# Optimization experiments

Measured on AMD Instinct MI355X. Metric: run time of the kernel, lower is better.

The kernel has to match this reference:

```python
import jax, jax.numpy as jnp
import numpy as np

N_CHUNKS = 4 * 28  # hardcoded 112 chunks in the original; chunk sizes are equal when N % 112 == 0


def setup_inputs() -> dict:
    key = jax.random.key(0)
    k1, k2, k3 = jax.random.split(key, 3)
    b, d, h, w = 8, 512, 28, 28  # N = b*h*w = 6272, divisible by 112
    x = jax.random.normal(k1, (b, d, h, w), dtype=jnp.float32)
    p_mu = jax.random.normal(k2, (b * h * w, d), dtype=jnp.float32)
    p_logvar = jax.random.normal(k3, (b * h * w, d), dtype=jnp.float32)
    return {"x": x, "p_mu": p_mu, "p_logvar": p_logvar}


def _club_loss(x, p_mu, p_logvar):
    # (b, d, h, w) -> (N, d) with N = b*h*w
    b, d, h, w = x.shape
    flat_x = jnp.transpose(x, (0, 2, 3, 1)).reshape(-1, d)  # (N, d)

    inv_ev = jnp.exp(-p_logvar)  # (N, d)

    # positive[i] = -0.5 * sum_d (x_i - mu_i)^2 / exp(logvar_i)
    positive = -0.5 * jnp.sum(jnp.square(flat_x - p_mu) * inv_ev, axis=-1)  # (N,)

    # negative[i] = -0.5 * mean_j sum_d (x_j - mu_i)^2 / exp(logvar_i)
    # Expand the square so the j-contraction becomes GEMMs (no (N,N,d) intermediate):
    #   D[i,j] = <x_j^2, inv_ev_i> - 2 <x_j, mu_i * inv_ev_i> + <mu_i^2, inv_ev_i>
    x2 = jnp.square(flat_x)                                   # (N, d)
    term_x2 = jnp.einsum('id,jd->ij', inv_ev, x2)             # (N_i, N_j)
    term_cross = jnp.einsum('id,jd->ij', p_mu * inv_ev, flat_x)
    term_mu2 = jnp.sum(jnp.square(p_mu) * inv_ev, axis=-1, keepdims=True)  # (N_i, 1)
    D = term_x2 - 2.0 * term_cross + term_mu2                 # (N_i, N_j)
    negative = -0.5 * jnp.mean(D, axis=1)                     # (N,)

    # Original averages each of the 112 equal-size chunks then averages the
    # chunk means, which equals the global mean for equal chunk sizes.
    return jnp.mean(positive - negative)


def reference(x, p_mu, p_logvar):
    return _club_loss(x, p_mu, p_logvar)
```

## Files before the change

### kernel.cpp

```cpp
#include <hip/hip_runtime.h>


#define Dd   512
#define HWs  784
#define Nn   6272
#define LSx  260


__global__ __launch_bounds__(256) void club_main(
    const float* __restrict__ x, const float* __restrict__ p_mu,
    const float* __restrict__ p_lv, float* __restrict__ ws)
{
    __shared__ __align__(16) float smem[16 * LSx + 16];

    const int t   = threadIdx.x;
    const int bid = blockIdx.x;
    const int ct  = bid & 1;
    const int ht  = (bid >> 1) % 49;
    const int b   = bid / 98;
    const int c0  = ct * 256;
    const int hw0 = ht * 16;
    const int rep = (bid >> 1) & 7;

    const int dx = t >> 2;
    const int g  = t & 3;
    const float* xb = x + ((size_t)(b * Dd + c0 + dx) * HWs + hw0 + 4 * g);
    const float4 x0 = *(const float4*)(xb);
    const float4 x1 = *(const float4*)(xb +  64 * HWs);
    const float4 x2 = *(const float4*)(xb + 128 * HWs);
    const float4 x3 = *(const float4*)(xb + 192 * HWs);

    const int r0 = b * HWs + hw0;
    const size_t mbase = (size_t)(r0 + (t >> 6)) * Dd + c0 + 4 * (t & 63);
    const float* mp = p_mu + mbase;
    const float* lp = p_lv + mbase;
    const float4 m0 = *(const float4*)(mp);
    const float4 m1 = *(const float4*)(mp + 2048);
    const float4 m2 = *(const float4*)(mp + 4096);
    const float4 m3 = *(const float4*)(mp + 6144);
    const float4 l0 = *(const float4*)(lp);
    const float4 l1 = *(const float4*)(lp + 2048);
    const float4 l2 = *(const float4*)(lp + 4096);
    const float4 l3 = *(const float4*)(lp + 6144);

    {
        const int rr = 4 * g;
#define XST(V, K) do {                                                \
        const int c = dx + 64 * (K);                                  \
        smem[(rr + 0) * LSx + c] = (V).x;                             \
        smem[(rr + 1) * LSx + c] = (V).y;                             \
        smem[(rr + 2) * LSx + c] = (V).z;                             \
        smem[(rr + 3) * LSx + c] = (V).w;                             \
    } while (0)
        XST(x0, 0); XST(x1, 1); XST(x2, 2); XST(x3, 3);
#undef XST
    }
    __syncthreads();

    float4 aI = {0,0,0,0}, aM = {0,0,0,0}, sX = {0,0,0,0}, sX2 = {0,0,0,0};
    float aP = 0.f, aM2 = 0.f;
    const int cc = 4 * (t & 63);
    const int rb = t >> 6;

#define ACC1(XV, MU, LV, F) do {                                      \
        const float iev = __expf(-(LV).F);                            \
        const float dd  = (XV).F - (MU).F;                            \
        aP += dd * dd * iev;                                          \
        aI.F += iev;                                                  \
        const float mi = (MU).F * iev;                                \
        aM.F += mi; aM2 += (MU).F * mi;                               \
        sX.F += (XV).F; sX2.F += (XV).F * (XV).F;                     \
    } while (0)
#define ACCROW(K, MU, LV) do {                                        \
        const float4 xv = *(const float4*)&smem[(rb + 4 * (K)) * LSx + cc]; \
        ACC1(xv, MU, LV, x); ACC1(xv, MU, LV, y);                     \
        ACC1(xv, MU, LV, z); ACC1(xv, MU, LV, w);                     \
    } while (0)
    ACCROW(0, m0, l0); ACCROW(1, m1, l1); ACCROW(2, m2, l2); ACCROW(3, m3, l3);
#undef ACCROW
#undef ACC1

    float4* red4 = (float4*)smem;
    float4 rI, rM, rX, rX2;
#define COLRED(SRC, DST) do {                                         \
        __syncthreads();                                              \
        red4[t] = (SRC);                                              \
        __syncthreads();                                              \
        if (t < 128) { float4 o = red4[t + 128];                      \
            red4[t].x += o.x; red4[t].y += o.y;                       \
            red4[t].z += o.z; red4[t].w += o.w; }                     \
        __syncthreads();                                              \
        if (t < 64) { float4 a = red4[t], o = red4[t + 64];           \
            (DST).x = a.x + o.x; (DST).y = a.y + o.y;                 \
            (DST).z = a.z + o.z; (DST).w = a.w + o.w; }               \
    } while (0)
    COLRED(aI, rI); COLRED(aM, rM); COLRED(sX, rX); COLRED(sX2, rX2);
#undef COLRED

#pragma unroll
    for (int off = 32; off > 0; off >>= 1) {
        aP  += __shfl_down(aP,  off);
        aM2 += __shfl_down(aM2, off);
    }
    __syncthreads();
    if ((t & 63) == 0) {
        smem[16 * LSx + (t >> 6)]     = aP;
        smem[16 * LSx + 8 + (t >> 6)] = aM2;
    }
    __syncthreads();

    if (t < 64) {
        const int c = c0 + 4 * t;
        float* wi = ws +         rep * Dd + c;
        float* wm = ws +  4096 + rep * Dd + c;
        float* wx = ws +  8192 + rep * Dd + c;
        float* w2 = ws + 12288 + rep * Dd + c;
        atomicAdd(wi + 0, rI.x); atomicAdd(wi + 1, rI.y);
        atomicAdd(wi + 2, rI.z); atomicAdd(wi + 3, rI.w);
        atomicAdd(wm + 0, rM.x); atomicAdd(wm + 1, rM.y);
        atomicAdd(wm + 2, rM.z); atomicAdd(wm + 3, rM.w);
        atomicAdd(wx + 0, rX.x); atomicAdd(wx + 1, rX.y);
        atomicAdd(wx + 2, rX.z); atomicAdd(wx + 3, rX.w);
        atomicAdd(w2 + 0, rX2.x); atomicAdd(w2 + 1, rX2.y);
        atomicAdd(w2 + 2, rX2.z); atomicAdd(w2 + 3, rX2.w);
    }
    if (t == 0) {
        double* wd = (double*)((char*)ws + 65536);
        atomicAdd(wd + rep, (double)(smem[16*LSx+0] + smem[16*LSx+1]
                                   + smem[16*LSx+2] + smem[16*LSx+3]));
        atomicAdd(wd + 8 + rep, (double)(smem[16*LSx+8] + smem[16*LSx+9]
                                       + smem[16*LSx+10] + smem[16*LSx+11]));
    }
}

__global__ __launch_bounds__(256) void club_fin(
    const float* __restrict__ ws, float* __restrict__ out)
{
    __shared__ double red[256];
    const int t = threadIdx.x;
    double acc = 0.0;
    for (int c = t; c < Dd; c += 256) {
        float inv = 0.f, muv = 0.f, sx = 0.f, sx2 = 0.f;
#pragma unroll
        for (int r = 0; r < 8; ++r) {
            inv += ws[r * Dd + c];
            muv += ws[4096 + r * Dd + c];
            sx  += ws[8192 + r * Dd + c];
            sx2 += ws[12288 + r * Dd + c];
        }
        acc += (double)sx2 * (double)inv - 2.0 * (double)sx * (double)muv;
    }
    red[t] = acc; __syncthreads();
    for (int s = 128; s > 0; s >>= 1) {
        if (t < s) red[t] += red[t + s];
        __syncthreads();
    }
    if (t == 0) {
        const double* wd = (const double*)((const char*)ws + 65536);
        double P = 0.0, M2 = 0.0;
#pragma unroll
        for (int r = 0; r < 8; ++r) { P += wd[r]; M2 += wd[8 + r]; }
        const double sumD = red[0] + (double)Nn * M2;
        out[0] = (float)((-0.5 / (double)Nn) * P
                       + (0.5 / ((double)Nn * (double)Nn)) * sumD);
    }
}

extern "C" void kernel_launch(void* const* d_in, const int* in_sizes, int n_in,
                              void* d_out, int out_size, void* d_ws, size_t ws_size,
                              hipStream_t stream) {
    const float* x    = (const float*)d_in[0];
    const float* p_mu = (const float*)d_in[1];
    const float* p_lv = (const float*)d_in[2];
    float* ws = (float*)d_ws;

    hipMemsetAsync(d_ws, 0, 65536 + 128, stream);

    club_main<<<784, 256, 0, stream>>>(x, p_mu, p_lv, ws);
    club_fin<<<1, 256, 0, stream>>>(ws, (float*)d_out);
}
```

Measured before the change: 102.3 us.

## Fuse finalize into main kernel via last-block counter and halve block count

Merges the separate finalize kernel into the main kernel: each block bumps an atomic counter after its partial sums, and the last block to finish runs the final reduction and writes the output. Each block now covers both channel halves for a 16-pixel tile, giving 392 blocks instead of 784 with double the loads in flight per thread. This removes one kernel launch and its dependency gap, at the cost of more registers and LDS per block and a serialized tail in the last block.

```diff
diff --git a/kernel.cpp b/kernel.cpp
--- a/kernel.cpp
+++ b/kernel.cpp
@@ -5,96 +5,119 @@
 #define HWs  784
 #define Nn   6272
 #define LSx  260
-
-
-__global__ __launch_bounds__(256) void club_main(
+#define NBLK 392
+
+
+__global__ __launch_bounds__(256) void club_all(
     const float* __restrict__ x, const float* __restrict__ p_mu,
-    const float* __restrict__ p_lv, float* __restrict__ ws)
+    const float* __restrict__ p_lv, float* __restrict__ ws,
+    float* __restrict__ out)
 {
-    __shared__ __align__(16) float smem[16 * LSx + 16];
+    __shared__ __align__(16) float smem[2 * 16 * LSx];
+    __shared__ float sbuf[16];
+    __shared__ int lastFlag;
 
     const int t   = threadIdx.x;
-    const int bid = blockIdx.x;
-    const int ct  = bid & 1;
-    const int ht  = (bid >> 1) % 49;
-    const int b   = bid / 98;
-    const int c0  = ct * 256;
+    const int j   = blockIdx.x;
+    const int b   = j / 49;
+    const int ht  = j % 49;
     const int hw0 = ht * 16;
-    const int rep = (bid >> 1) & 7;
-
-    const int dx = t >> 2;
-    const int g  = t & 3;
-    const float* xb = x + ((size_t)(b * Dd + c0 + dx) * HWs + hw0 + 4 * g);
-    const float4 x0 = *(const float4*)(xb);
-    const float4 x1 = *(const float4*)(xb +  64 * HWs);
-    const float4 x2 = *(const float4*)(xb + 128 * HWs);
-    const float4 x3 = *(const float4*)(xb + 192 * HWs);
-
-    const int r0 = b * HWs + hw0;
-    const size_t mbase = (size_t)(r0 + (t >> 6)) * Dd + c0 + 4 * (t & 63);
-    const float* mp = p_mu + mbase;
-    const float* lp = p_lv + mbase;
-    const float4 m0 = *(const float4*)(mp);
-    const float4 m1 = *(const float4*)(mp + 2048);
-    const float4 m2 = *(const float4*)(mp + 4096);
-    const float4 m3 = *(const float4*)(mp + 6144);
-    const float4 l0 = *(const float4*)(lp);
-    const float4 l1 = *(const float4*)(lp + 2048);
-    const float4 l2 = *(const float4*)(lp + 4096);
-    const float4 l3 = *(const float4*)(lp + 6144);
-
-    {
-        const int rr = 4 * g;
-#define XST(V, K) do {                                                \
-        const int c = dx + 64 * (K);                                  \
-        smem[(rr + 0) * LSx + c] = (V).x;                             \
-        smem[(rr + 1) * LSx + c] = (V).y;                             \
-        smem[(rr + 2) * LSx + c] = (V).z;                             \
-        smem[(rr + 3) * LSx + c] = (V).w;                             \
-    } while (0)
-        XST(x0, 0); XST(x1, 1); XST(x2, 2); XST(x3, 3);
+    const int r0  = b * HWs + hw0;
+    const int rep = j & 7;
+
+    const int dx = t >> 2, g = t & 3;
+    const float* xb0 = x + ((size_t)(b * Dd + dx) * HWs + hw0 + 4 * g);
+    const float4 A0 = *(const float4*)(xb0);
+    const float4 A1 = *(const float4*)(xb0 +  64 * HWs);
+    const float4 A2 = *(const float4*)(xb0 + 128 * HWs);
+    const float4 A3 = *(const float4*)(xb0 + 192 * HWs);
+    const float* xb1 = xb0 + 256 * HWs;
+    const float4 B0 = *(const float4*)(xb1);
+    const float4 B1 = *(const float4*)(xb1 +  64 * HWs);
+    const float4 B2 = *(const float4*)(xb1 + 128 * HWs);
+    const float4 B3 = *(const float4*)(xb1 + 192 * HWs);
+
+    const size_t mb0 = (size_t)(r0 + (t >> 6)) * Dd + 4 * (t & 63);
+    const float4 M00 = *(const float4*)(p_mu + mb0);
+    const float4 M01 = *(const float4*)(p_mu + mb0 + 2048);
+    const float4 M02 = *(const float4*)(p_mu + mb0 + 4096);
+    const float4 M03 = *(const float4*)(p_mu + mb0 + 6144);
+    const float4 L00 = *(const float4*)(p_lv + mb0);
+    const float4 L01 = *(const float4*)(p_lv + mb0 + 2048);
+    const float4 L02 = *(const float4*)(p_lv + mb0 + 4096);
+    const float4 L03 = *(const float4*)(p_lv + mb0 + 6144);
+
+#define XST(V, HALF, K) do {                                           \
+        const int c_ = dx + 64 * (K);                                  \
+        float* s_ = smem + (HALF) * 16 * LSx + (4 * g) * LSx + c_;     \
+        s_[0 * LSx] = (V).x; s_[1 * LSx] = (V).y;                      \
+        s_[2 * LSx] = (V).z; s_[3 * LSx] = (V).w;                      \
+    } while (0)
+    XST(A0, 0, 0); XST(A1, 0, 1); XST(A2, 0, 2); XST(A3, 0, 3);
+    XST(B0, 1, 0); XST(B1, 1, 1); XST(B2, 1, 2); XST(B3, 1, 3);
 #undef XST
-    }
-    __syncthreads();
-
-    float4 aI = {0,0,0,0}, aM = {0,0,0,0}, sX = {0,0,0,0}, sX2 = {0,0,0,0};
-    float aP = 0.f, aM2 = 0.f;
+
+    const size_t mb1 = mb0 + 256;
+    const float4 M10 = *(const float4*)(p_mu + mb1);
+    const float4 M11 = *(const float4*)(p_mu + mb1 + 2048);
+    const float4 M12 = *(const float4*)(p_mu + mb1 + 4096);
+    const float4 M13 = *(const float4*)(p_mu + mb1 + 6144);
+    const float4 L10 = *(const float4*)(p_lv + mb1);
+    const float4 L11 = *(const float4*)(p_lv + mb1 + 2048);
+    const float4 L12 = *(const float4*)(p_lv + mb1 + 4096);
+    const float4 L13 = *(const float4*)(p_lv + mb1 + 6144);
+
+    __syncthreads();
+
     const int cc = 4 * (t & 63);
     const int rb = t >> 6;
-
-#define ACC1(XV, MU, LV, F) do {                                      \
-        const float iev = __expf(-(LV).F);                            \
-        const float dd  = (XV).F - (MU).F;                            \
-        aP += dd * dd * iev;                                          \
-        aI.F += iev;                                                  \
-        const float mi = (MU).F * iev;                                \
-        aM.F += mi; aM2 += (MU).F * mi;                               \
-        sX.F += (XV).F; sX2.F += (XV).F * (XV).F;                     \
-    } while (0)
-#define ACCROW(K, MU, LV) do {                                        \
-        const float4 xv = *(const float4*)&smem[(rb + 4 * (K)) * LSx + cc]; \
-        ACC1(xv, MU, LV, x); ACC1(xv, MU, LV, y);                     \
-        ACC1(xv, MU, LV, z); ACC1(xv, MU, LV, w);                     \
-    } while (0)
-    ACCROW(0, m0, l0); ACCROW(1, m1, l1); ACCROW(2, m2, l2); ACCROW(3, m3, l3);
+    float4 aI0 = {0,0,0,0}, aM0 = {0,0,0,0}, sX0 = {0,0,0,0}, s20 = {0,0,0,0};
+    float4 aI1 = {0,0,0,0}, aM1 = {0,0,0,0}, sX1 = {0,0,0,0}, s21 = {0,0,0,0};
+    float aP = 0.f, aM2 = 0.f;
+
+#define ACC1(XV, MU, LV, F, AI, AM, SX, S2) do {                       \
+        const float iev = __expf(-(LV).F);                             \
+        const float dd  = (XV).F - (MU).F;                             \
+        aP += dd * dd * iev;                                           \
+        (AI).F += iev;                                                 \
+        const float mi = (MU).F * iev;                                 \
+        (AM).F += mi; aM2 += (MU).F * mi;                              \
+        (SX).F += (XV).F; (S2).F += (XV).F * (XV).F;                   \
+    } while (0)
+#define ACCROW(HALF, K, MU, LV, AI, AM, SX, S2) do {                   \
+        const float4 xv = *(const float4*)&smem[(HALF)*16*LSx + (rb + 4*(K))*LSx + cc]; \
+        ACC1(xv, MU, LV, x, AI, AM, SX, S2);                           \
+        ACC1(xv, MU, LV, y, AI, AM, SX, S2);                           \
+        ACC1(xv, MU, LV, z, AI, AM, SX, S2);                           \
+        ACC1(xv, MU, LV, w, AI, AM, SX, S2);                           \
+    } while (0)
+    ACCROW(0, 0, M00, L00, aI0, aM0, sX0, s20);
+    ACCROW(0, 1, M01, L01, aI0, aM0, sX0, s20);
+    ACCROW(0, 2, M02, L02, aI0, aM0, sX0, s20);
+    ACCROW(0, 3, M03, L03, aI0, aM0, sX0, s20);
+    ACCROW(1, 0, M10, L10, aI1, aM1, sX1, s21);
+    ACCROW(1, 1, M11, L11, aI1, aM1, sX1, s21);
+    ACCROW(1, 2, M12, L12, aI1, aM1, sX1, s21);
+    ACCROW(1, 3, M13, L13, aI1, aM1, sX1, s21);
 #undef ACCROW
 #undef ACC1
 
     float4* red4 = (float4*)smem;
-    float4 rI, rM, rX, rX2;
-#define COLRED(SRC, DST) do {                                         \
-        __syncthreads();                                              \
-        red4[t] = (SRC);                                              \
-        __syncthreads();                                              \
-        if (t < 128) { float4 o = red4[t + 128];                      \
-            red4[t].x += o.x; red4[t].y += o.y;                       \
-            red4[t].z += o.z; red4[t].w += o.w; }                     \
-        __syncthreads();                                              \
-        if (t < 64) { float4 a = red4[t], o = red4[t + 64];           \
-            (DST).x = a.x + o.x; (DST).y = a.y + o.y;                 \
-            (DST).z = a.z + o.z; (DST).w = a.w + o.w; }               \
-    } while (0)
-    COLRED(aI, rI); COLRED(aM, rM); COLRED(sX, rX); COLRED(sX2, rX2);
+    float4 rI0, rM0, rX0, r20, rI1, rM1, rX1, r21;
+#define COLRED(SRC, DST) do {                                          \
+        __syncthreads();                                               \
+        red4[t] = (SRC);                                               \
+        __syncthreads();                                               \
+        if (t < 128) { float4 o = red4[t + 128];                       \
+            red4[t].x += o.x; red4[t].y += o.y;                        \
+            red4[t].z += o.z; red4[t].w += o.w; }                      \
+        __syncthreads();                                               \
+        if (t < 64) { float4 a = red4[t], o = red4[t + 64];            \
+            (DST).x = a.x + o.x; (DST).y = a.y + o.y;                  \
+            (DST).z = a.z + o.z; (DST).w = a.w + o.w; }                \
+    } while (0)
+    COLRED(aI0, rI0); COLRED(aM0, rM0); COLRED(sX0, rX0); COLRED(s20, r20);
+    COLRED(aI1, rI1); COLRED(aM1, rM1); COLRED(sX1, rX1); COLRED(s21, r21);
 #undef COLRED
 
 #pragma unroll
@@ -103,64 +126,65 @@
         aM2 += __shfl_down(aM2, off);
     }
     __syncthreads();
-    if ((t & 63) == 0) {
-        smem[16 * LSx + (t >> 6)]     = aP;
-        smem[16 * LSx + 8 + (t >> 6)] = aM2;
-    }
+    if ((t & 63) == 0) { sbuf[t >> 6] = aP; sbuf[8 + (t >> 6)] = aM2; }
     __syncthreads();
 
     if (t < 64) {
-        const int c = c0 + 4 * t;
-        float* wi = ws +         rep * Dd + c;
-        float* wm = ws +  4096 + rep * Dd + c;
-        float* wx = ws +  8192 + rep * Dd + c;
-        float* w2 = ws + 12288 + rep * Dd + c;
-        atomicAdd(wi + 0, rI.x); atomicAdd(wi + 1, rI.y);
-        atomicAdd(wi + 2, rI.z); atomicAdd(wi + 3, rI.w);
-        atomicAdd(wm + 0, rM.x); atomicAdd(wm + 1, rM.y);
-        atomicAdd(wm + 2, rM.z); atomicAdd(wm + 3, rM.w);
-        atomicAdd(wx + 0, rX.x); atomicAdd(wx + 1, rX.y);
-        atomicAdd(wx + 2, rX.z); atomicAdd(wx + 3, rX.w);
-        atomicAdd(w2 + 0, rX2.x); atomicAdd(w2 + 1, rX2.y);
-        atomicAdd(w2 + 2, rX2.z); atomicAdd(w2 + 3, rX2.w);
+#define ATOM4(OFF, C, V) do {                                          \
+        float* p_ = ws + (OFF) + rep * Dd + (C);                       \
+        atomicAdd(p_ + 0, (V).x); atomicAdd(p_ + 1, (V).y);            \
+        atomicAdd(p_ + 2, (V).z); atomicAdd(p_ + 3, (V).w);            \
+    } while (0)
+        ATOM4(0,     4 * t,       rI0); ATOM4(0,     256 + 4 * t, rI1);
+        ATOM4(4096,  4 * t,       rM0); ATOM4(4096,  256 + 4 * t, rM1);
+        ATOM4(8192,  4 * t,       rX0); ATOM4(8192,  256 + 4 * t, rX1);
+        ATOM4(12288, 4 * t,       r20); ATOM4(12288, 256 + 4 * t, r21);
+#undef ATOM4
     }
     if (t == 0) {
         double* wd = (double*)((char*)ws + 65536);
-        atomicAdd(wd + rep, (double)(smem[16*LSx+0] + smem[16*LSx+1]
-                                   + smem[16*LSx+2] + smem[16*LSx+3]));
-        atomicAdd(wd + 8 + rep, (double)(smem[16*LSx+8] + smem[16*LSx+9]
-                                       + smem[16*LSx+10] + smem[16*LSx+11]));
-    }
-}
-
-__global__ __launch_bounds__(256) void club_fin(
-    const float* __restrict__ ws, float* __restrict__ out)
-{
-    __shared__ double red[256];
-    const int t = threadIdx.x;
-    double acc = 0.0;
-    for (int c = t; c < Dd; c += 256) {
-        float inv = 0.f, muv = 0.f, sx = 0.f, sx2 = 0.f;
+        atomicAdd(wd + rep,     (double)(sbuf[0] + sbuf[1] + sbuf[2] + sbuf[3]));
+        atomicAdd(wd + 8 + rep, (double)(sbuf[8] + sbuf[9] + sbuf[10] + sbuf[11]));
+    }
+
+    if (t == 0) {
+        __threadfence();
+        unsigned* ctr = (unsigned*)((char*)ws + 65664);
+        lastFlag = (atomicAdd(ctr, 1u) == NBLK - 1);
+    }
+    __syncthreads();
+    if (!lastFlag) return;
+
+    __threadfence();
+    double* redd = (double*)smem;
+    double dc = 0.0;
+#pragma unroll
+    for (int half = 0; half < 2; ++half) {
+        const int c = t + 256 * half;
+        double sI = 0.0, sM = 0.0, sX = 0.0, s2 = 0.0;
 #pragma unroll
         for (int r = 0; r < 8; ++r) {
-            inv += ws[r * Dd + c];
-            muv += ws[4096 + r * Dd + c];
-            sx  += ws[8192 + r * Dd + c];
-            sx2 += ws[12288 + r * Dd + c];
+            sI += (double)__hip_atomic_load(ws +         r * Dd + c, __ATOMIC_RELAXED, __HIP_MEMORY_SCOPE_AGENT);
+            sM += (double)__hip_atomic_load(ws +  4096 + r * Dd + c, __ATOMIC_RELAXED, __HIP_MEMORY_SCOPE_AGENT);
+            sX += (double)__hip_atomic_load(ws +  8192 + r * Dd + c, __ATOMIC_RELAXED, __HIP_MEMORY_SCOPE_AGENT);
+            s2 += (double)__hip_atomic_load(ws + 12288 + r * Dd + c, __ATOMIC_RELAXED, __HIP_MEMORY_SCOPE_AGENT);
         }
-        acc += (double)sx2 * (double)inv - 2.0 * (double)sx * (double)muv;
-    }
-    red[t] = acc; __syncthreads();
+        dc += s2 * sI - 2.0 * sX * sM;
+    }
+    redd[t] = dc; __syncthreads();
     for (int s = 128; s > 0; s >>= 1) {
-        if (t < s) red[t] += red[t + s];
+        if (t < s) redd[t] += redd[t + s];
         __syncthreads();
     }
     if (t == 0) {
-        const double* wd = (const double*)((const char*)ws + 65536);
+        double* wd = (double*)((char*)ws + 65536);
         double P = 0.0, M2 = 0.0;
 #pragma unroll
-        for (int r = 0; r < 8; ++r) { P += wd[r]; M2 += wd[8 + r]; }
-        const double sumD = red[0] + (double)Nn * M2;
+        for (int r = 0; r < 8; ++r) {
+            P  += __hip_atomic_load(wd + r,     __ATOMIC_RELAXED, __HIP_MEMORY_SCOPE_AGENT);
+            M2 += __hip_atomic_load(wd + 8 + r, __ATOMIC_RELAXED, __HIP_MEMORY_SCOPE_AGENT);
+        }
+        const double sumD = redd[0] + (double)Nn * M2;
         out[0] = (float)((-0.5 / (double)Nn) * P
                        + (0.5 / ((double)Nn * (double)Nn)) * sumD);
     }
@@ -174,8 +198,6 @@
     const float* p_lv = (const float*)d_in[2];
     float* ws = (float*)d_ws;
 
-    hipMemsetAsync(d_ws, 0, 65536 + 128, stream);
-
-    club_main<<<784, 256, 0, stream>>>(x, p_mu, p_lv, ws);
-    club_fin<<<1, 256, 0, stream>>>(ws, (float*)d_out);
+    hipMemsetAsync(d_ws, 0, 65668, stream);
+    club_all<<<NBLK, 256, 0, stream>>>(x, p_mu, p_lv, ws, (float*)d_out);
 }
```

Result: no change. 102.6 us (+0.3%).
